# Performance work log

Measured on AMD Instinct MI355X. Metric: run time of the kernel, lower is better.

The kernel has to match this reference:

```python
import jax, jax.numpy as jnp
import numpy as np

N_NODES = 50000
N_EDGES = 800000
D_IN = 128
HC = 128
D_OUT = 128
BN_EPS = 1e-5
RRELU_SLOPE = (1.0 / 8.0 + 1.0 / 3.0) / 2.0  # RReLU eval mode: (lower+upper)/2 = 11/48


def setup_inputs() -> dict:
    key = jax.random.key(0)
    ks = jax.random.split(key, 10)
    s_in = 1.0 / np.sqrt(D_IN)
    s_hc = 1.0 / np.sqrt(HC)
    return {
        "x": jax.random.normal(ks[0], (N_NODES, D_IN), jnp.float32),
        "edge_index": jax.random.randint(ks[1], (2, N_EDGES), 0, N_NODES),
        "edge_attr": jax.random.uniform(ks[2], (N_EDGES,), jnp.float32),
        # conv1: GraphConv(D_IN -> HC): lin_rel (with bias) + lin_root (no bias)
        "W1_rel": jax.random.normal(ks[3], (HC, D_IN), jnp.float32) * s_in,
        "b1": jnp.zeros((HC,), jnp.float32),
        "W1_root": jax.random.normal(ks[4], (HC, D_IN), jnp.float32) * s_in,
        # bn1 affine params
        "gamma": jnp.ones((HC,), jnp.float32),
        "beta": jnp.zeros((HC,), jnp.float32),
        # conv2: GraphConv(HC -> D_OUT)
        "W2_rel": jax.random.normal(ks[5], (D_OUT, HC), jnp.float32) * s_hc,
        "b2": jnp.zeros((D_OUT,), jnp.float32),
        "W2_root": jax.random.normal(ks[6], (D_OUT, HC), jnp.float32) * s_hc,
    }


def graph_conv(x, src, tgt, edge_w, W_rel, b_rel, W_root):
    # message: edge_weight * x[src]; aggregate: scatter-add into target nodes
    msg = x[src] * edge_w[:, None]                                   # [E, F]
    agg = jax.ops.segment_sum(msg, tgt, num_segments=x.shape[0])     # [N, F]
    return agg @ W_rel.T + b_rel + x @ W_root.T                      # [N, F_out]


def reference(x, edge_index, edge_attr, W1_rel, b1, W1_root, gamma, beta, W2_rel, b2, W2_root):
    src, tgt = edge_index[0], edge_index[1]
    h = graph_conv(x, src, tgt, edge_attr, W1_rel, b1, W1_root)      # [N, HC]
    # BatchNorm1d (training mode: biased batch stats over node dim)
    mean = h.mean(axis=0)
    var = h.var(axis=0)
    h = (h - mean) * jax.lax.rsqrt(var + BN_EPS) * gamma + beta
    # RReLU (deterministic eval slope)
    h = jnp.where(h >= 0, h, h * RRELU_SLOPE)
    return graph_conv(h, src, tgt, edge_attr, W2_rel, b2, W2_root)   # [N, D_OUT]
```

## Files before the change

### kernel.cpp

```cpp
#include <hip/hip_runtime.h>

#define N_NODES 50000
#define N_EDGES 800000
#define F 128
#define BN_EPS 1e-5f
#define SLOPE 0.22916666666666666f

#define NBKT 196
#define BKT_CAP 8192
#define P1_CHUNK 4096
#define P1_EPB 16
#define P1_BLKS 196
#define CASTX_BLKS 6250
#define CASTW_BLKS 64
#define REC_CAP 1152608
#define N_TILES 3125
#define GG_GRID 1024

typedef __attribute__((ext_vector_type(8))) short bf16x8;
typedef __attribute__((ext_vector_type(4))) float f32x4;
typedef unsigned long long u64;

__device__ __forceinline__ float bf2f(ushort u) {
    union { uint i; float f; } v; v.i = (uint)u << 16; return v.f;
}
__device__ __forceinline__ ushort f2bf(float f) {
    union { float f; uint i; } v; v.f = f;
    uint r = v.i + 0x7fffu + ((v.i >> 16) & 1u);
    return (ushort)(r >> 16);
}

__global__ __launch_bounds__(256) void s1p_k(const int* __restrict__ src,
        const int* __restrict__ tgt, const float* __restrict__ ew,
        int* __restrict__ bcur, u64* __restrict__ stg,
        const float* __restrict__ x, ushort* __restrict__ xb,
        const float* __restrict__ W1r, const float* __restrict__ W1t,
        const float* __restrict__ W2r, const float* __restrict__ W2t,
        ushort* __restrict__ wb) {
    const int b = blockIdx.x;
    if (b >= P1_BLKS) {
        if (b < P1_BLKS + CASTX_BLKS) {
            int i = (b - P1_BLKS) * 256 + threadIdx.x;
            float4 v = reinterpret_cast<const float4*>(x)[i];
            ushort4 o;
            o.x = f2bf(v.x); o.y = f2bf(v.y); o.z = f2bf(v.z); o.w = f2bf(v.w);
            reinterpret_cast<ushort4*>(xb)[i] = o;
        } else {
            int i = (b - P1_BLKS - CASTX_BLKS) * 256 + threadIdx.x;
            int m = i >> 12;
            int j = i & 4095;
            const float* sp = (m == 0) ? W1r : (m == 1) ? W1t : (m == 2) ? W2r : W2t;
            float4 v = reinterpret_cast<const float4*>(sp)[j];
            ushort4 o;
            o.x = f2bf(v.x); o.y = f2bf(v.y); o.z = f2bf(v.z); o.w = f2bf(v.w);
            reinterpret_cast<ushort4*>(wb)[i] = o;
        }
        return;
    }
    __shared__ uint cnt[256];
    __shared__ uint base[256];
    __shared__ uint lcur[256];
    __shared__ uint gbase[256];
    __shared__ u64 lrec[P1_CHUNK];

    const int e0 = b * P1_CHUNK;
    const int nE = min(P1_CHUNK, N_EDGES - e0);
    cnt[threadIdx.x] = 0;
    __syncthreads();

    u64 myrec[P1_EPB];
    bool myok[P1_EPB];
#pragma unroll
    for (int k = 0; k < P1_EPB; ++k) {
        int idx = threadIdx.x + (k << 8);
        bool ok = idx < nE;
        myok[k] = ok;
        if (ok) {
            int e = e0 + idx;
            uint t = (uint)tgt[e];
            uint lo = (uint)(ushort)src[e] | ((uint)f2bf(ew[e]) << 16);
            myrec[k] = (u64)lo | ((u64)t << 32);
            atomicAdd(&cnt[t >> 8], 1u);
        }
    }
    __syncthreads();
    uint v = cnt[threadIdx.x];
    base[threadIdx.x] = v;
    __syncthreads();
    for (int o = 1; o < 256; o <<= 1) {
        uint t = (threadIdx.x >= (unsigned)o) ? base[threadIdx.x - o] : 0;
        __syncthreads();
        base[threadIdx.x] += t;
        __syncthreads();
    }
    uint excl = base[threadIdx.x] - v;
    base[threadIdx.x] = excl;
    lcur[threadIdx.x] = excl;
    if (threadIdx.x < NBKT && v > 0)
        gbase[threadIdx.x] = (uint)threadIdx.x * BKT_CAP +
                             (uint)atomicAdd(&bcur[threadIdx.x], (int)v);
    __syncthreads();
#pragma unroll
    for (int k = 0; k < P1_EPB; ++k) {
        if (myok[k]) {
            uint bb = (uint)(myrec[k] >> 40);
            uint slot = atomicAdd(&lcur[bb], 1u);
            lrec[slot] = myrec[k];
        }
    }
    __syncthreads();
    for (int s = threadIdx.x; s < nE; s += 256) {
        u64 r = lrec[s];
        uint bb = (uint)(r >> 40);
        stg[gbase[bb] + ((uint)s - base[bb])] = r;
    }
}

__global__ __launch_bounds__(256) void sort2_k(const int* __restrict__ bcur,
        const u64* __restrict__ stg, uint* __restrict__ recs, int2* __restrict__ rng) {
    __shared__ int lcnt[256];
    __shared__ int lcur[256];
    __shared__ int sc[256];
    __shared__ int fbase_s;
    const int b = blockIdx.x;
    const int tid = threadIdx.x;

    int cnt_t = (tid < NBKT) ? bcur[tid] : 0;
    int stride_t = (tid < NBKT) ? (((cnt_t + 7) & ~7) + 1792) : 0;
    sc[tid] = stride_t;
    lcnt[tid] = 0;
    __syncthreads();
    for (int o = 1; o < 256; o <<= 1) {
        int t = (tid >= o) ? sc[tid - o] : 0;
        __syncthreads();
        sc[tid] += t;
        __syncthreads();
    }
    if (tid == b) fbase_s = sc[tid] - stride_t;
    __syncthreads();
    const int fbase = fbase_s;
    const int cnt = bcur[b];
    const u64* sb = stg + (size_t)b * BKT_CAP;

    for (int i = tid; i < cnt; i += 256)
        atomicAdd(&lcnt[(int)(sb[i] >> 32) & 255], 1);
    __syncthreads();
    int myc = lcnt[tid];
    int myp = (myc + 7) & ~7;
    sc[tid] = myp;
    __syncthreads();
    for (int o = 1; o < 256; o <<= 1) {
        int t = (tid >= o) ? sc[tid - o] : 0;
        __syncthreads();
        sc[tid] += t;
        __syncthreads();
    }
    int excl = sc[tid] - myp;
    int node = b * 256 + tid;
    if (node < N_NODES) rng[node] = make_int2(fbase + excl, fbase + excl + myp);
    lcur[tid] = fbase + excl;
    __syncthreads();
    for (int i = tid; i < cnt; i += 256) {
        u64 r = sb[i];
        int n = (int)(r >> 32) & 255;
        int p = atomicAdd(&lcur[n], 1);
        recs[p] = (uint)r;
    }
}

__global__ __launch_bounds__(256) void gg_k(const ushort* __restrict__ featb,
        const int2* __restrict__ rng, const uint* __restrict__ recs,
        const ushort* __restrict__ Wr, const ushort* __restrict__ Wt,
        const float* __restrict__ bias, float* __restrict__ out,
        ushort* __restrict__ outh, float* __restrict__ S, float* __restrict__ S2,
        int layer1) {
    __shared__ ushort As[2][16][136];

    const int lane = threadIdx.x & 63;
    const int wave = threadIdx.x >> 6;
    const int quad = lane >> 4;
    const int l16 = lane & 15;
    const int cb = wave * 32;
    const int lane2 = lane * 2;

    bf16x8 bR[2][4], bT[2][4];
#pragma unroll
    for (int t = 0; t < 2; ++t)
#pragma unroll
        for (int s = 0; s < 4; ++s) {
            int col = cb + t * 16 + l16;
            int k0 = s * 32 + quad * 8;
            bR[t][s] = *reinterpret_cast<const bf16x8*>(Wr + col * F + k0);
            bT[t][s] = *reinterpret_cast<const bf16x8*>(Wt + col * F + k0);
        }
    const float bias0 = bias[cb + l16];
    const float bias1 = bias[cb + 16 + l16];

    float s0 = 0.f, q0 = 0.f, s1 = 0.f, q1 = 0.f;
    int dbuf = 0;

    for (int tile = blockIdx.x; tile < N_TILES; tile += GG_GRID) {
#pragma unroll
        for (int g = 0; g < 4; ++g) {
            int node = tile * 16 + wave * 4 + g;
            int2 r = rng[node];
            float a0 = 0.f, a1 = 0.f;
            for (int p = r.x; p < r.y; p += 8) {
                uint4 ra = *reinterpret_cast<const uint4*>(recs + p);
                uint4 rb = *reinterpret_cast<const uint4*>(recs + p + 4);
                uint u0 = *reinterpret_cast<const uint*>(featb + (size_t)(ra.x & 0xffffu) * F + lane2);
                uint u1 = *reinterpret_cast<const uint*>(featb + (size_t)(ra.y & 0xffffu) * F + lane2);
                uint u2 = *reinterpret_cast<const uint*>(featb + (size_t)(ra.z & 0xffffu) * F + lane2);
                uint u3 = *reinterpret_cast<const uint*>(featb + (size_t)(ra.w & 0xffffu) * F + lane2);
                uint u4 = *reinterpret_cast<const uint*>(featb + (size_t)(rb.x & 0xffffu) * F + lane2);
                uint u5 = *reinterpret_cast<const uint*>(featb + (size_t)(rb.y & 0xffffu) * F + lane2);
                uint u6 = *reinterpret_cast<const uint*>(featb + (size_t)(rb.z & 0xffffu) * F + lane2);
                uint u7 = *reinterpret_cast<const uint*>(featb + (size_t)(rb.w & 0xffffu) * F + lane2);
                float w0 = bf2f((ushort)(ra.x >> 16)), w1 = bf2f((ushort)(ra.y >> 16));
                float w2 = bf2f((ushort)(ra.z >> 16)), w3 = bf2f((ushort)(ra.w >> 16));
                float w4 = bf2f((ushort)(rb.x >> 16)), w5 = bf2f((ushort)(rb.y >> 16));
                float w6 = bf2f((ushort)(rb.z >> 16)), w7 = bf2f((ushort)(rb.w >> 16));
                a0 += w0 * bf2f((ushort)u0) + w1 * bf2f((ushort)u1)
                    + w2 * bf2f((ushort)u2) + w3 * bf2f((ushort)u3)
                    + w4 * bf2f((ushort)u4) + w5 * bf2f((ushort)u5)
                    + w6 * bf2f((ushort)u6) + w7 * bf2f((ushort)u7);
                a1 += w0 * bf2f((ushort)(u0 >> 16)) + w1 * bf2f((ushort)(u1 >> 16))
                    + w2 * bf2f((ushort)(u2 >> 16)) + w3 * bf2f((ushort)(u3 >> 16))
                    + w4 * bf2f((ushort)(u4 >> 16)) + w5 * bf2f((ushort)(u5 >> 16))
                    + w6 * bf2f((ushort)(u6 >> 16)) + w7 * bf2f((ushort)(u7 >> 16));
            }
            *reinterpret_cast<uint*>(&As[dbuf][wave * 4 + g][lane2]) =
                (uint)f2bf(a0) | ((uint)f2bf(a1) << 16);
        }
        __syncthreads();
        const int row0 = tile * 16;
        bf16x8 aR0 = *reinterpret_cast<const bf16x8*>(&As[dbuf][l16][quad * 8]);
        bf16x8 aR1 = *reinterpret_cast<const bf16x8*>(&As[dbuf][l16][quad * 8 + 32]);
        bf16x8 aR2 = *reinterpret_cast<const bf16x8*>(&As[dbuf][l16][quad * 8 + 64]);
        bf16x8 aR3 = *reinterpret_cast<const bf16x8*>(&As[dbuf][l16][quad * 8 + 96]);
        const ushort* tA = featb + (size_t)(row0 + l16) * F + quad * 8;
        bf16x8 aT0 = *reinterpret_cast<const bf16x8*>(tA);
        bf16x8 aT1 = *reinterpret_cast<const bf16x8*>(tA + 32);
        bf16x8 aT2 = *reinterpret_cast<const bf16x8*>(tA + 64);
        bf16x8 aT3 = *reinterpret_cast<const bf16x8*>(tA + 96);

        f32x4 acc0 = {0.f, 0.f, 0.f, 0.f};
        f32x4 acc1 = {0.f, 0.f, 0.f, 0.f};
        acc0 = __builtin_amdgcn_mfma_f32_16x16x32_bf16(aR0, bR[0][0], acc0, 0, 0, 0);
        acc1 = __builtin_amdgcn_mfma_f32_16x16x32_bf16(aR0, bR[1][0], acc1, 0, 0, 0);
        acc0 = __builtin_amdgcn_mfma_f32_16x16x32_bf16(aR1, bR[0][1], acc0, 0, 0, 0);
        acc1 = __builtin_amdgcn_mfma_f32_16x16x32_bf16(aR1, bR[1][1], acc1, 0, 0, 0);
        acc0 = __builtin_amdgcn_mfma_f32_16x16x32_bf16(aR2, bR[0][2], acc0, 0, 0, 0);
        acc1 = __builtin_amdgcn_mfma_f32_16x16x32_bf16(aR2, bR[1][2], acc1, 0, 0, 0);
        acc0 = __builtin_amdgcn_mfma_f32_16x16x32_bf16(aR3, bR[0][3], acc0, 0, 0, 0);
        acc1 = __builtin_amdgcn_mfma_f32_16x16x32_bf16(aR3, bR[1][3], acc1, 0, 0, 0);
        acc0 = __builtin_amdgcn_mfma_f32_16x16x32_bf16(aT0, bT[0][0], acc0, 0, 0, 0);
        acc1 = __builtin_amdgcn_mfma_f32_16x16x32_bf16(aT0, bT[1][0], acc1, 0, 0, 0);
        acc0 = __builtin_amdgcn_mfma_f32_16x16x32_bf16(aT1, bT[0][1], acc0, 0, 0, 0);
        acc1 = __builtin_amdgcn_mfma_f32_16x16x32_bf16(aT1, bT[1][1], acc1, 0, 0, 0);
        acc0 = __builtin_amdgcn_mfma_f32_16x16x32_bf16(aT2, bT[0][2], acc0, 0, 0, 0);
        acc1 = __builtin_amdgcn_mfma_f32_16x16x32_bf16(aT2, bT[1][2], acc1, 0, 0, 0);
        acc0 = __builtin_amdgcn_mfma_f32_16x16x32_bf16(aT3, bT[0][3], acc0, 0, 0, 0);
        acc1 = __builtin_amdgcn_mfma_f32_16x16x32_bf16(aT3, bT[1][3], acc1, 0, 0, 0);

        const int r0 = row0 + quad * 4;
        if (layer1) {
#pragma unroll
            for (int g = 0; g < 4; ++g) {
                float v0 = acc0[g] + bias0;
                float v1 = acc1[g] + bias1;
                outh[(r0 + g) * F + cb + l16] = f2bf(v0);
                outh[(r0 + g) * F + cb + 16 + l16] = f2bf(v1);
                s0 += v0; q0 += v0 * v0;
                s1 += v1; q1 += v1 * v1;
            }
        } else {
#pragma unroll
            for (int g = 0; g < 4; ++g) {
                out[(r0 + g) * F + cb + l16] = acc0[g] + bias0;
                out[(r0 + g) * F + cb + 16 + l16] = acc1[g] + bias1;
            }
        }
        dbuf ^= 1;
    }

    if (layer1) {
        s0 += __shfl_down(s0, 32); s0 += __shfl_down(s0, 16);
        q0 += __shfl_down(q0, 32); q0 += __shfl_down(q0, 16);
        s1 += __shfl_down(s1, 32); s1 += __shfl_down(s1, 16);
        q1 += __shfl_down(q1, 32); q1 += __shfl_down(q1, 16);
        if (lane < 16) {
            unsafeAtomicAdd(&S[cb + lane], s0);
            unsafeAtomicAdd(&S2[cb + lane], q0);
            unsafeAtomicAdd(&S[cb + 16 + lane], s1);
            unsafeAtomicAdd(&S2[cb + 16 + lane], q1);
        }
    }
}

__global__ __launch_bounds__(256) void norm_act_k(const ushort* __restrict__ hraw,
        const float* __restrict__ S, const float* __restrict__ S2,
        const float* __restrict__ gamma, const float* __restrict__ beta,
        ushort* __restrict__ hb) {
    __shared__ float sc_s[128], sh_s[128];
    if (threadIdx.x < 128) {
        int j = threadIdx.x;
        float mean = S[j] * (1.f / N_NODES);
        float var = S2[j] * (1.f / N_NODES) - mean * mean;
        float inv = rsqrtf(var + BN_EPS);
        float sc = gamma[j] * inv;
        sc_s[j] = sc;
        sh_s[j] = beta[j] - mean * sc;
    }
    __syncthreads();
    int i = blockIdx.x * 256 + threadIdx.x;
    int cbase = (i & 31) * 4;
    uint2 u = reinterpret_cast<const uint2*>(hraw)[i];
    float4 v = make_float4(bf2f((ushort)u.x), bf2f((ushort)(u.x >> 16)),
                           bf2f((ushort)u.y), bf2f((ushort)(u.y >> 16)));
    float4 sc = *reinterpret_cast<const float4*>(&sc_s[cbase]);
    float4 sh = *reinterpret_cast<const float4*>(&sh_s[cbase]);
    v.x = v.x * sc.x + sh.x;
    v.y = v.y * sc.y + sh.y;
    v.z = v.z * sc.z + sh.z;
    v.w = v.w * sc.w + sh.w;
    v.x = v.x >= 0.f ? v.x : v.x * SLOPE;
    v.y = v.y >= 0.f ? v.y : v.y * SLOPE;
    v.z = v.z >= 0.f ? v.z : v.z * SLOPE;
    v.w = v.w >= 0.f ? v.w : v.w * SLOPE;
    uint2 o;
    o.x = (uint)f2bf(v.x) | ((uint)f2bf(v.y) << 16);
    o.y = (uint)f2bf(v.z) | ((uint)f2bf(v.w) << 16);
    reinterpret_cast<uint2*>(hb)[i] = o;
}

extern "C" void kernel_launch(void* const* d_in, const int* in_sizes, int n_in,
                              void* d_out, int out_size, void* d_ws, size_t ws_size,
                              hipStream_t stream) {
    const float* x     = (const float*)d_in[0];
    const int*   ei    = (const int*)d_in[1];
    const float* ea    = (const float*)d_in[2];
    const float* W1r   = (const float*)d_in[3];
    const float* b1    = (const float*)d_in[4];
    const float* W1t   = (const float*)d_in[5];
    const float* gamma = (const float*)d_in[6];
    const float* beta  = (const float*)d_in[7];
    const float* W2r   = (const float*)d_in[8];
    const float* b2    = (const float*)d_in[9];
    const float* W2t   = (const float*)d_in[10];
    float* out = (float*)d_out;

    char* ws = (char*)d_ws;
    size_t off = 0;
    u64*    stg   = (u64*)(ws + off);    off += (size_t)NBKT * BKT_CAP * 8;
    ushort* featb = (ushort*)(ws + off); off += (size_t)N_NODES * F * 2;
    uint*   recs  = (uint*)(ws + off);   off += (size_t)REC_CAP * 4;
    int*    bcur  = (int*)(ws + off);    off += 256 * 4;
    float*  S     = (float*)(ws + off);  off += 128 * 4;
    float*  S2    = (float*)(ws + off);  off += 128 * 4;
    int2*   rng   = (int2*)(ws + off);   off += (size_t)N_NODES * 8;
    ushort* wb    = (ushort*)(ws + off); off += 4 * 16384 * 2;
    ushort* hraw  = (ushort*)d_out;

    const int* srcp = ei;
    const int* tgtp = ei + N_EDGES;

    hipMemsetAsync(recs, 0, (size_t)REC_CAP * 4 + 256 * 4 + 256 * 4, stream);
    s1p_k<<<P1_BLKS + CASTX_BLKS + CASTW_BLKS, 256, 0, stream>>>(
        srcp, tgtp, ea, bcur, stg, x, featb, W1r, W1t, W2r, W2t, wb);
    sort2_k<<<NBKT, 256, 0, stream>>>(bcur, stg, recs, rng);

    gg_k<<<GG_GRID, 256, 0, stream>>>(featb, rng, recs, wb, wb + 16384, b1,
                                      out, hraw, S, S2, 1);
    norm_act_k<<<CASTX_BLKS, 256, 0, stream>>>(hraw, S, S2, gamma, beta, featb);
    gg_k<<<GG_GRID, 256, 0, stream>>>(featb, rng, recs, wb + 32768, wb + 49152, b2,
                                      out, hraw, S, S2, 0);
}
```

Measured before the change: 248.5 us.

## Pad per-node edge lists to 16, sort by source, interleave four nodes' gathers

The CSR build now stages each bucket's records in shared memory. It pads every node's edge list to a multiple of 16 with a minimum of 16, insertion-sorts each node's records by source index, and writes the padded buckets out contiguously, so the large memset of recs is no longer needed. The gather loop in gg_k now processes four nodes per wave together: it runs 16 unconditional records per node first, then a predicated tail, which raises the number of independent loads in flight and makes source access more local. The costs are more padding work on zero-weight records, a serial per-thread insertion sort in sort2_k, and larger shared memory use.

```diff
diff --git a/kernel.cpp b/kernel.cpp
--- a/kernel.cpp
+++ b/kernel.cpp
@@ -13,7 +13,8 @@
 #define P1_BLKS 196
 #define CASTX_BLKS 6250
 #define CASTW_BLKS 64
-#define REC_CAP 1152608
+#define BKT_FINAL_CAP 8704
+#define REC_CAP 1606016
 #define N_TILES 3125
 #define GG_GRID 1024
 
@@ -119,14 +120,16 @@
 __global__ __launch_bounds__(256) void sort2_k(const int* __restrict__ bcur,
         const u64* __restrict__ stg, uint* __restrict__ recs, int2* __restrict__ rng) {
     __shared__ int lcnt[256];
+    __shared__ int loff[256];
     __shared__ int lcur[256];
     __shared__ int sc[256];
     __shared__ int fbase_s;
+    __shared__ uint lrec[BKT_FINAL_CAP];
     const int b = blockIdx.x;
     const int tid = threadIdx.x;
 
     int cnt_t = (tid < NBKT) ? bcur[tid] : 0;
-    int stride_t = (tid < NBKT) ? (((cnt_t + 7) & ~7) + 1792) : 0;
+    int stride_t = (tid < NBKT) ? (((cnt_t + 15) & ~15) + 4096) : 0;
     sc[tid] = stride_t;
     lcnt[tid] = 0;
     __syncthreads();
@@ -145,8 +148,11 @@
     for (int i = tid; i < cnt; i += 256)
         atomicAdd(&lcnt[(int)(sb[i] >> 32) & 255], 1);
     __syncthreads();
+    const int node = b * 256 + tid;
     int myc = lcnt[tid];
-    int myp = (myc + 7) & ~7;
+    int myp = (myc + 15) & ~15;
+    if (myp == 0) myp = 16;
+    if (node >= N_NODES) myp = 0;
     sc[tid] = myp;
     __syncthreads();
     for (int o = 1; o < 256; o <<= 1) {
@@ -155,17 +161,35 @@
         sc[tid] += t;
         __syncthreads();
     }
-    int excl = sc[tid] - myp;
-    int node = b * 256 + tid;
-    if (node < N_NODES) rng[node] = make_int2(fbase + excl, fbase + excl + myp);
-    lcur[tid] = fbase + excl;
+    const int myoff = sc[tid] - myp;
+    const int ptot = sc[255];
+    loff[tid] = myoff;
+    lcur[tid] = myoff;
+    if (node < N_NODES) rng[node] = make_int2(fbase + myoff, fbase + myoff + myp);
+    for (int i = tid; i < ptot; i += 256) lrec[i] = 0;
     __syncthreads();
     for (int i = tid; i < cnt; i += 256) {
         u64 r = sb[i];
         int n = (int)(r >> 32) & 255;
         int p = atomicAdd(&lcur[n], 1);
-        recs[p] = (uint)r;
-    }
+        lrec[p] = (uint)r;
+    }
+    __syncthreads();
+    {
+        int s0_ = loff[tid];
+        for (int i = 1; i < myc; ++i) {
+            uint key = lrec[s0_ + i];
+            ushort ks = (ushort)key;
+            int j = i - 1;
+            while (j >= 0 && (ushort)lrec[s0_ + j] > ks) {
+                lrec[s0_ + j + 1] = lrec[s0_ + j];
+                --j;
+            }
+            lrec[s0_ + j + 1] = key;
+        }
+    }
+    __syncthreads();
+    for (int i = tid; i < ptot; i += 256) recs[fbase + i] = lrec[i];
 }
 
 __global__ __launch_bounds__(256) void gg_k(const ushort* __restrict__ featb,
@@ -200,40 +224,129 @@
     int dbuf = 0;
 
     for (int tile = blockIdx.x; tile < N_TILES; tile += GG_GRID) {
-#pragma unroll
-        for (int g = 0; g < 4; ++g) {
-            int node = tile * 16 + wave * 4 + g;
-            int2 r = rng[node];
-            float a0 = 0.f, a1 = 0.f;
-            for (int p = r.x; p < r.y; p += 8) {
-                uint4 ra = *reinterpret_cast<const uint4*>(recs + p);
-                uint4 rb = *reinterpret_cast<const uint4*>(recs + p + 4);
-                uint u0 = *reinterpret_cast<const uint*>(featb + (size_t)(ra.x & 0xffffu) * F + lane2);
-                uint u1 = *reinterpret_cast<const uint*>(featb + (size_t)(ra.y & 0xffffu) * F + lane2);
-                uint u2 = *reinterpret_cast<const uint*>(featb + (size_t)(ra.z & 0xffffu) * F + lane2);
-                uint u3 = *reinterpret_cast<const uint*>(featb + (size_t)(ra.w & 0xffffu) * F + lane2);
-                uint u4 = *reinterpret_cast<const uint*>(featb + (size_t)(rb.x & 0xffffu) * F + lane2);
-                uint u5 = *reinterpret_cast<const uint*>(featb + (size_t)(rb.y & 0xffffu) * F + lane2);
-                uint u6 = *reinterpret_cast<const uint*>(featb + (size_t)(rb.z & 0xffffu) * F + lane2);
-                uint u7 = *reinterpret_cast<const uint*>(featb + (size_t)(rb.w & 0xffffu) * F + lane2);
-                float w0 = bf2f((ushort)(ra.x >> 16)), w1 = bf2f((ushort)(ra.y >> 16));
-                float w2 = bf2f((ushort)(ra.z >> 16)), w3 = bf2f((ushort)(ra.w >> 16));
-                float w4 = bf2f((ushort)(rb.x >> 16)), w5 = bf2f((ushort)(rb.y >> 16));
-                float w6 = bf2f((ushort)(rb.z >> 16)), w7 = bf2f((ushort)(rb.w >> 16));
-                a0 += w0 * bf2f((ushort)u0) + w1 * bf2f((ushort)u1)
-                    + w2 * bf2f((ushort)u2) + w3 * bf2f((ushort)u3)
-                    + w4 * bf2f((ushort)u4) + w5 * bf2f((ushort)u5)
-                    + w6 * bf2f((ushort)u6) + w7 * bf2f((ushort)u7);
-                a1 += w0 * bf2f((ushort)(u0 >> 16)) + w1 * bf2f((ushort)(u1 >> 16))
-                    + w2 * bf2f((ushort)(u2 >> 16)) + w3 * bf2f((ushort)(u3 >> 16))
-                    + w4 * bf2f((ushort)(u4 >> 16)) + w5 * bf2f((ushort)(u5 >> 16))
-                    + w6 * bf2f((ushort)(u6 >> 16)) + w7 * bf2f((ushort)(u7 >> 16));
-            }
-            *reinterpret_cast<uint*>(&As[dbuf][wave * 4 + g][lane2]) =
-                (uint)f2bf(a0) | ((uint)f2bf(a1) << 16);
-        }
-        __syncthreads();
         const int row0 = tile * 16;
+        const int nodeb = row0 + wave * 4;
+        int2 r0_ = rng[nodeb + 0];
+        int2 r1_ = rng[nodeb + 1];
+        int2 r2_ = rng[nodeb + 2];
+        int2 r3_ = rng[nodeb + 3];
+        float ax0 = 0.f, ay0 = 0.f, ax1 = 0.f, ay1 = 0.f;
+        float ax2 = 0.f, ay2 = 0.f, ax3 = 0.f, ay3 = 0.f;
+
+#pragma unroll 1
+        for (int k = 0; k < 16; k += 4) {
+            uint4 qa = *reinterpret_cast<const uint4*>(recs + r0_.x + k);
+            uint4 qb = *reinterpret_cast<const uint4*>(recs + r1_.x + k);
+            uint4 qc = *reinterpret_cast<const uint4*>(recs + r2_.x + k);
+            uint4 qd = *reinterpret_cast<const uint4*>(recs + r3_.x + k);
+            uint u0 = *reinterpret_cast<const uint*>(featb + (size_t)(qa.x & 0xffffu) * F + lane2);
+            uint u1 = *reinterpret_cast<const uint*>(featb + (size_t)(qa.y & 0xffffu) * F + lane2);
+            uint u2 = *reinterpret_cast<const uint*>(featb + (size_t)(qa.z & 0xffffu) * F + lane2);
+            uint u3 = *reinterpret_cast<const uint*>(featb + (size_t)(qa.w & 0xffffu) * F + lane2);
+            uint u4 = *reinterpret_cast<const uint*>(featb + (size_t)(qb.x & 0xffffu) * F + lane2);
+            uint u5 = *reinterpret_cast<const uint*>(featb + (size_t)(qb.y & 0xffffu) * F + lane2);
+            uint u6 = *reinterpret_cast<const uint*>(featb + (size_t)(qb.z & 0xffffu) * F + lane2);
+            uint u7 = *reinterpret_cast<const uint*>(featb + (size_t)(qb.w & 0xffffu) * F + lane2);
+            uint u8 = *reinterpret_cast<const uint*>(featb + (size_t)(qc.x & 0xffffu) * F + lane2);
+            uint u9 = *reinterpret_cast<const uint*>(featb + (size_t)(qc.y & 0xffffu) * F + lane2);
+            uint uA = *reinterpret_cast<const uint*>(featb + (size_t)(qc.z & 0xffffu) * F + lane2);
+            uint uB = *reinterpret_cast<const uint*>(featb + (size_t)(qc.w & 0xffffu) * F + lane2);
+            uint uC = *reinterpret_cast<const uint*>(featb + (size_t)(qd.x & 0xffffu) * F + lane2);
+            uint uD = *reinterpret_cast<const uint*>(featb + (size_t)(qd.y & 0xffffu) * F + lane2);
+            uint uE = *reinterpret_cast<const uint*>(featb + (size_t)(qd.z & 0xffffu) * F + lane2);
+            uint uF = *reinterpret_cast<const uint*>(featb + (size_t)(qd.w & 0xffffu) * F + lane2);
+            float w0 = bf2f((ushort)(qa.x >> 16)), w1 = bf2f((ushort)(qa.y >> 16));
+            float w2 = bf2f((ushort)(qa.z >> 16)), w3 = bf2f((ushort)(qa.w >> 16));
+            float w4 = bf2f((ushort)(qb.x >> 16)), w5 = bf2f((ushort)(qb.y >> 16));
+            float w6 = bf2f((ushort)(qb.z >> 16)), w7 = bf2f((ushort)(qb.w >> 16));
+            float w8 = bf2f((ushort)(qc.x >> 16)), w9 = bf2f((ushort)(qc.y >> 16));
+            float wA = bf2f((ushort)(qc.z >> 16)), wB = bf2f((ushort)(qc.w >> 16));
+            float wC = bf2f((ushort)(qd.x >> 16)), wD = bf2f((ushort)(qd.y >> 16));
+            float wE = bf2f((ushort)(qd.z >> 16)), wF = bf2f((ushort)(qd.w >> 16));
+            ax0 += w0 * bf2f((ushort)u0) + w1 * bf2f((ushort)u1)
+                 + w2 * bf2f((ushort)u2) + w3 * bf2f((ushort)u3);
+            ay0 += w0 * bf2f((ushort)(u0 >> 16)) + w1 * bf2f((ushort)(u1 >> 16))
+                 + w2 * bf2f((ushort)(u2 >> 16)) + w3 * bf2f((ushort)(u3 >> 16));
+            ax1 += w4 * bf2f((ushort)u4) + w5 * bf2f((ushort)u5)
+                 + w6 * bf2f((ushort)u6) + w7 * bf2f((ushort)u7);
+            ay1 += w4 * bf2f((ushort)(u4 >> 16)) + w5 * bf2f((ushort)(u5 >> 16))
+                 + w6 * bf2f((ushort)(u6 >> 16)) + w7 * bf2f((ushort)(u7 >> 16));
+            ax2 += w8 * bf2f((ushort)u8) + w9 * bf2f((ushort)u9)
+                 + wA * bf2f((ushort)uA) + wB * bf2f((ushort)uB);
+            ay2 += w8 * bf2f((ushort)(u8 >> 16)) + w9 * bf2f((ushort)(u9 >> 16))
+                 + wA * bf2f((ushort)(uA >> 16)) + wB * bf2f((ushort)(uB >> 16));
+            ax3 += wC * bf2f((ushort)uC) + wD * bf2f((ushort)uD)
+                 + wE * bf2f((ushort)uE) + wF * bf2f((ushort)uF);
+            ay3 += wC * bf2f((ushort)(uC >> 16)) + wD * bf2f((ushort)(uD >> 16))
+                 + wE * bf2f((ushort)(uE >> 16)) + wF * bf2f((ushort)(uF >> 16));
+        }
+        int mx = max(max(r0_.y - r0_.x, r1_.y - r1_.x),
+                     max(r2_.y - r2_.x, r3_.y - r3_.x));
+#pragma unroll 1
+        for (int k = 16; k < mx; k += 4) {
+            if (r0_.x + k < r0_.y) {
+                uint4 q = *reinterpret_cast<const uint4*>(recs + r0_.x + k);
+                uint u0 = *reinterpret_cast<const uint*>(featb + (size_t)(q.x & 0xffffu) * F + lane2);
+                uint u1 = *reinterpret_cast<const uint*>(featb + (size_t)(q.y & 0xffffu) * F + lane2);
+                uint u2 = *reinterpret_cast<const uint*>(featb + (size_t)(q.z & 0xffffu) * F + lane2);
+                uint u3 = *reinterpret_cast<const uint*>(featb + (size_t)(q.w & 0xffffu) * F + lane2);
+                float w0 = bf2f((ushort)(q.x >> 16)), w1 = bf2f((ushort)(q.y >> 16));
+                float w2 = bf2f((ushort)(q.z >> 16)), w3 = bf2f((ushort)(q.w >> 16));
+                ax0 += w0 * bf2f((ushort)u0) + w1 * bf2f((ushort)u1)
+                     + w2 * bf2f((ushort)u2) + w3 * bf2f((ushort)u3);
+                ay0 += w0 * bf2f((ushort)(u0 >> 16)) + w1 * bf2f((ushort)(u1 >> 16))
+                     + w2 * bf2f((ushort)(u2 >> 16)) + w3 * bf2f((ushort)(u3 >> 16));
+            }
+            if (r1_.x + k < r1_.y) {
+                uint4 q = *reinterpret_cast<const uint4*>(recs + r1_.x + k);
+                uint u0 = *reinterpret_cast<const uint*>(featb + (size_t)(q.x & 0xffffu) * F + lane2);
+                uint u1 = *reinterpret_cast<const uint*>(featb + (size_t)(q.y & 0xffffu) * F + lane2);
+                uint u2 = *reinterpret_cast<const uint*>(featb + (size_t)(q.z & 0xffffu) * F + lane2);
+                uint u3 = *reinterpret_cast<const uint*>(featb + (size_t)(q.w & 0xffffu) * F + lane2);
+                float w0 = bf2f((ushort)(q.x >> 16)), w1 = bf2f((ushort)(q.y >> 16));
+                float w2 = bf2f((ushort)(q.z >> 16)), w3 = bf2f((ushort)(q.w >> 16));
+                ax1 += w0 * bf2f((ushort)u0) + w1 * bf2f((ushort)u1)
+                     + w2 * bf2f((ushort)u2) + w3 * bf2f((ushort)u3);
+                ay1 += w0 * bf2f((ushort)(u0 >> 16)) + w1 * bf2f((ushort)(u1 >> 16))
+                     + w2 * bf2f((ushort)(u2 >> 16)) + w3 * bf2f((ushort)(u3 >> 16));
+            }
+            if (r2_.x + k < r2_.y) {
+                uint4 q = *reinterpret_cast<const uint4*>(recs + r2_.x + k);
+                uint u0 = *reinterpret_cast<const uint*>(featb + (size_t)(q.x & 0xffffu) * F + lane2);
+                uint u1 = *reinterpret_cast<const uint*>(featb + (size_t)(q.y & 0xffffu) * F + lane2);
+                uint u2 = *reinterpret_cast<const uint*>(featb + (size_t)(q.z & 0xffffu) * F + lane2);
+                uint u3 = *reinterpret_cast<const uint*>(featb + (size_t)(q.w & 0xffffu) * F + lane2);
+                float w0 = bf2f((ushort)(q.x >> 16)), w1 = bf2f((ushort)(q.y >> 16));
+                float w2 = bf2f((ushort)(q.z >> 16)), w3 = bf2f((ushort)(q.w >> 16));
+                ax2 += w0 * bf2f((ushort)u0) + w1 * bf2f((ushort)u1)
+                     + w2 * bf2f((ushort)u2) + w3 * bf2f((ushort)u3);
+                ay2 += w0 * bf2f((ushort)(u0 >> 16)) + w1 * bf2f((ushort)(u1 >> 16))
+                     + w2 * bf2f((ushort)(u2 >> 16)) + w3 * bf2f((ushort)(u3 >> 16));
+            }
+            if (r3_.x + k < r3_.y) {
+                uint4 q = *reinterpret_cast<const uint4*>(recs + r3_.x + k);
+                uint u0 = *reinterpret_cast<const uint*>(featb + (size_t)(q.x & 0xffffu) * F + lane2);
+                uint u1 = *reinterpret_cast<const uint*>(featb + (size_t)(q.y & 0xffffu) * F + lane2);
+                uint u2 = *reinterpret_cast<const uint*>(featb + (size_t)(q.z & 0xffffu) * F + lane2);
+                uint u3 = *reinterpret_cast<const uint*>(featb + (size_t)(q.w & 0xffffu) * F + lane2);
+                float w0 = bf2f((ushort)(q.x >> 16)), w1 = bf2f((ushort)(q.y >> 16));
+                float w2 = bf2f((ushort)(q.z >> 16)), w3 = bf2f((ushort)(q.w >> 16));
+                ax3 += w0 * bf2f((ushort)u0) + w1 * bf2f((ushort)u1)
+                     + w2 * bf2f((ushort)u2) + w3 * bf2f((ushort)u3);
+                ay3 += w0 * bf2f((ushort)(u0 >> 16)) + w1 * bf2f((ushort)(u1 >> 16))
+                     + w2 * bf2f((ushort)(u2 >> 16)) + w3 * bf2f((ushort)(u3 >> 16));
+            }
+        }
+
+        *reinterpret_cast<uint*>(&As[dbuf][wave * 4 + 0][lane2]) =
+            (uint)f2bf(ax0) | ((uint)f2bf(ay0) << 16);
+        *reinterpret_cast<uint*>(&As[dbuf][wave * 4 + 1][lane2]) =
+            (uint)f2bf(ax1) | ((uint)f2bf(ay1) << 16);
+        *reinterpret_cast<uint*>(&As[dbuf][wave * 4 + 2][lane2]) =
+            (uint)f2bf(ax2) | ((uint)f2bf(ay2) << 16);
+        *reinterpret_cast<uint*>(&As[dbuf][wave * 4 + 3][lane2]) =
+            (uint)f2bf(ax3) | ((uint)f2bf(ay3) << 16);
+        __syncthreads();
         bf16x8 aR0 = *reinterpret_cast<const bf16x8*>(&As[dbuf][l16][quad * 8]);
         bf16x8 aR1 = *reinterpret_cast<const bf16x8*>(&As[dbuf][l16][quad * 8 + 32]);
         bf16x8 aR2 = *reinterpret_cast<const bf16x8*>(&As[dbuf][l16][quad * 8 + 64]);
@@ -365,7 +478,7 @@
     const int* srcp = ei;
     const int* tgtp = ei + N_EDGES;
 
-    hipMemsetAsync(recs, 0, (size_t)REC_CAP * 4 + 256 * 4 + 256 * 4, stream);
+    hipMemsetAsync(bcur, 0, 256 * 4 + 256 * 4, stream);
     s1p_k<<<P1_BLKS + CASTX_BLKS + CASTW_BLKS, 256, 0, stream>>>(
         srcp, tgtp, ea, bcur, stg, x, featb, W1r, W1t, W2r, W2t, wb);
     sort2_k<<<NBKT, 256, 0, stream>>>(bcur, stg, recs, rng);
```

Result: slower. 335.2 us (+34.9%).
